# Performance work log

Hardware: AMD Instinct MI355X
Metric: run time of the kernel (lower is better)

## Reference

```python
import jax, jax.numpy as jnp
import numpy as np


def _gru(x, Wih, Whh, bih, bhh):
    # PyTorch GRU cell math, batch=1: x [S, IN], Wih [3H, IN], Whh [3H, H]
    H = Whh.shape[1]
    def step(h, xt):
        gi = Wih @ xt + bih
        gh = Whh @ h + bhh
        i_r, i_z, i_n = jnp.split(gi, 3)
        h_r, h_z, h_n = jnp.split(gh, 3)
        r = jax.nn.sigmoid(i_r + h_r)
        z = jax.nn.sigmoid(i_z + h_z)
        n = jnp.tanh(i_n + r * h_n)
        hn = (1.0 - z) * n + z * h
        return hn, hn
    _, hs = jax.lax.scan(step, jnp.zeros((H,), x.dtype), x)
    return hs  # [S, H]


def setup_inputs() -> dict:
    key = jax.random.key(0)
    ks = jax.random.split(key, 18)
    LOC, TIM, UID = 100000, 48, 5000
    DL, DT, DU, H = 256, 32, 64, 256
    SEQ, NH, TOT, TGT = 2048, 4096, 16384, 1024
    IN = DL + DT  # 288
    s = 0.02
    return {
        "loc": jax.random.randint(ks[0], (SEQ,), 0, LOC),
        "tim": jax.random.randint(ks[1], (SEQ,), 0, TIM),
        "history_loc": jax.random.randint(ks[2], (TOT,), 0, LOC),
        "history_tim": jax.random.randint(ks[3], (TOT,), 0, TIM),
        "history_count": jnp.full((NH,), TOT // NH, dtype=jnp.int32),
        "uid": jax.random.randint(ks[4], (1,), 0, UID),
        "target_len": TGT,
        "emb_loc": jax.random.normal(ks[5], (LOC, DL), jnp.float32) * s,
        "emb_tim": jax.random.normal(ks[6], (TIM, DT), jnp.float32) * s,
        "emb_uid": jax.random.normal(ks[7], (UID, DU), jnp.float32) * s,
        "W_attn": jax.random.normal(ks[8], (2 * H, IN), jnp.float32) * s,
        "b_attn": jnp.zeros((2 * H,), jnp.float32),
        "Wih_f": jax.random.normal(ks[9], (3 * H, IN), jnp.float32) * s,
        "Whh_f": jax.random.normal(ks[10], (3 * H, H), jnp.float32) * s,
        "bih_f": jnp.zeros((3 * H,), jnp.float32),
        "bhh_f": jnp.zeros((3 * H,), jnp.float32),
        "Wih_b": jax.random.normal(ks[11], (3 * H, IN), jnp.float32) * s,
        "Whh_b": jax.random.normal(ks[12], (3 * H, H), jnp.float32) * s,
        "bih_b": jnp.zeros((3 * H,), jnp.float32),
        "bhh_b": jnp.zeros((3 * H,), jnp.float32),
        "Wf": jax.random.normal(ks[13], (LOC, 4 * H + DU), jnp.float32) * s,
        "bf": jnp.zeros((LOC,), jnp.float32),
    }


def reference(loc, tim, history_loc, history_tim, history_count, uid, target_len,
              emb_loc, emb_tim, emb_uid, W_attn, b_attn,
              Wih_f, Whh_f, bih_f, bhh_f, Wih_b, Whh_b, bih_b, bhh_b, Wf, bf):
    counts = np.asarray(jax.device_get(history_count))  # static ragged structure
    n = counts.shape[0]
    seg = jnp.asarray(np.repeat(np.arange(n), counts))
    offs = jnp.asarray(np.concatenate([[0], np.cumsum(counts)[:-1]]))

    # current trajectory embedding [S, IN] (dropout is identity in eval)
    x = jnp.concatenate([emb_loc[loc], emb_tim[tim]], axis=1)

    # ragged segment mean of history loc embeddings; first tim embedding per group
    le = emb_loc[history_loc]  # [TOT, DL]
    loc_mean = jax.ops.segment_sum(le, seg, num_segments=n) / counts.astype(le.dtype)[:, None]
    tim_first = emb_tim[history_tim][offs]  # [n, DT]
    history = jnp.tanh(jnp.concatenate([loc_mean, tim_first], axis=1) @ W_attn.T + b_attn)  # [n, 2H]

    # bidirectional GRU, batch 1
    hf = _gru(x, Wih_f, Whh_f, bih_f, bhh_f)
    hb = _gru(x[::-1], Wih_b, Whh_b, bih_b, bhh_b)[::-1]
    out_state = jnp.concatenate([hf, hb], axis=1)  # [S, 2H]

    q = out_state[-target_len:]                      # [T, 2H]
    attn = jax.nn.softmax(q @ history.T, axis=1)     # dot-product attention
    context = attn @ history                         # [T, 2H]

    uid_emb = jnp.broadcast_to(emb_uid[uid], (target_len, emb_uid.shape[1]))
    out = jnp.concatenate([q, context, uid_emb], axis=1)  # [T, 4H+DU]
    return jax.nn.log_softmax(out @ Wf.T + bf, axis=1)    # [T, LOC]
```

## Files before the change

kernel.cpp:

```cpp
#include <hip/hip_runtime.h>
#include <hip/hip_bf16.h>
#include <stdint.h>

typedef unsigned int uint;
typedef unsigned short ushort;

#define SEQ   2048
#define TGT   1024
#define HDIM  256
#define IN3   288
#define G3    768
#define NHIST 4096
#define DL    256
#define DT    32
#define DU    64
#define NLOC  100000
#define DOUT  1088

typedef short short8 __attribute__((ext_vector_type(8)));
typedef float floatx4 __attribute__((ext_vector_type(4)));
typedef float float4v __attribute__((ext_vector_type(4)));
typedef ushort ushort8v __attribute__((ext_vector_type(8)));
typedef _Float16 half8v __attribute__((ext_vector_type(8)));

__device__ __forceinline__ ushort f2bf(float f) {
  uint u = __builtin_bit_cast(uint, f);
  u += 0x7FFFu + ((u >> 16) & 1u);
  return (ushort)(u >> 16);
}

__global__ void k_pack_whh(const float* __restrict__ whf, const float* __restrict__ whb,
                           uint4* __restrict__ wpack) {
  int idx = blockIdx.x * 256 + threadIdx.x;
  int dir = idx / 24576;
  int r = idx - dir * 24576;
  int wave = r / 3072;
  int r2 = r - wave * 3072;
  int rt = r2 / 512;
  int r3 = r2 - rt * 512;
  int kt = r3 / 64;
  int lane = r3 - kt * 64;
  int row = wave * 96 + rt * 16 + (lane & 15);
  int kb = kt * 32 + (lane >> 4) * 8;
  const float* W = dir ? whb : whf;
  const float* src = W + (size_t)row * 256 + kb;
  half8v h;
  #pragma unroll
  for (int j = 0; j < 8; ++j) h[j] = (_Float16)src[j];
  wpack[idx] = __builtin_bit_cast(uint4, h);
}

__global__ void k_embed_x(const int* __restrict__ loc, const int* __restrict__ tim,
                          const float* __restrict__ emb_loc, const float* __restrict__ emb_tim,
                          ushort* __restrict__ xb) {
  int t = blockIdx.x;
  int tid = threadIdx.x;
  int l = loc[t], m = tim[t];
  if (tid < 256) xb[(size_t)t * IN3 + tid] = f2bf(emb_loc[(size_t)l * DL + tid]);
  if (tid < 32)  xb[(size_t)t * IN3 + 256 + tid] = f2bf(emb_tim[m * DT + tid]);
}

__global__ void k_scan(const int* __restrict__ counts, int* __restrict__ offs) {
  __shared__ int sd[1024];
  int tid = threadIdx.x;
  int base = tid * 4;
  int c0 = counts[base], c1 = counts[base + 1], c2 = counts[base + 2], c3 = counts[base + 3];
  int tot = c0 + c1 + c2 + c3;
  sd[tid] = tot;
  __syncthreads();
  int val = tot;
  for (int off = 1; off < 1024; off <<= 1) {
    int v = (tid >= off) ? sd[tid - off] : 0;
    __syncthreads();
    val += v;
    sd[tid] = val;
    __syncthreads();
  }
  int excl = val - tot;
  offs[base] = excl;
  offs[base + 1] = excl + c0;
  offs[base + 2] = excl + c0 + c1;
  offs[base + 3] = excl + c0 + c1 + c2;
}

__global__ void k_hin(const int* __restrict__ hloc, const int* __restrict__ htim,
                      const int* __restrict__ counts, const int* __restrict__ offs,
                      const float* __restrict__ emb_loc, const float* __restrict__ emb_tim,
                      ushort* __restrict__ hin) {
  int i = blockIdx.x;
  int tid = threadIdx.x;
  int off = offs[i], cnt = counts[i];
  float4v s = {0.f, 0.f, 0.f, 0.f};
  for (int e = 0; e < cnt; ++e) {
    int l = hloc[off + e];
    const float4v* row = (const float4v*)(emb_loc + (size_t)l * DL);
    s += row[tid];
  }
  float inv = 1.f / (float)cnt;
  size_t b = (size_t)i * IN3 + tid * 4;
  hin[b + 0] = f2bf(s[0] * inv);
  hin[b + 1] = f2bf(s[1] * inv);
  hin[b + 2] = f2bf(s[2] * inv);
  hin[b + 3] = f2bf(s[3] * inv);
  if (tid < 32) {
    int ht = htim[off];
    hin[(size_t)i * IN3 + 256 + tid] = f2bf(emb_tim[ht * DT + tid]);
  }
}

template<bool BF32, int ACT>
__global__ __launch_bounds__(256, 2)
void k_gemm(const ushort* __restrict__ A, const void* __restrict__ Bv,
            const float* __restrict__ bias, float* __restrict__ C,
            int M, int N, int K) {
  __shared__ __align__(16) ushort As[128 * 40];
  __shared__ __align__(16) ushort Bs[128 * 40];
  const int tid = threadIdx.x;
  const int m0 = blockIdx.x * 128;
  const int n0 = blockIdx.y * 128;
  const int wave = tid >> 6, lane = tid & 63;
  const int wm = (wave & 1) << 6, wn = (wave >> 1) << 6;
  const int r16 = lane & 15, kq = lane >> 4;
  floatx4 acc[4][4];
  for (int i = 0; i < 4; i++)
    for (int j = 0; j < 4; j++)
      acc[i][j] = (floatx4){0.f, 0.f, 0.f, 0.f};
  const int srow = tid >> 1;
  const int scol = (tid & 1) << 4;
  const bool bok = (n0 + srow) < N;
  for (int k0 = 0; k0 < K; k0 += 32) {
    const ushort* ap = A + (size_t)(m0 + srow) * K + k0 + scol;
    uint4 a0 = *(const uint4*)ap;
    uint4 a1 = *(const uint4*)(ap + 8);
    *(uint4*)&As[srow * 40 + scol] = a0;
    *(uint4*)&As[srow * 40 + scol + 8] = a1;
    if (BF32) {
      const float* bp = (const float*)Bv + (size_t)(n0 + srow) * K + k0 + scol;
      float4v b0 = {0,0,0,0}, b1 = {0,0,0,0}, b2 = {0,0,0,0}, b3 = {0,0,0,0};
      if (bok) {
        b0 = ((const float4v*)bp)[0];
        b1 = ((const float4v*)bp)[1];
        b2 = ((const float4v*)bp)[2];
        b3 = ((const float4v*)bp)[3];
      }
      ushort8v v0, v1;
      for (int j = 0; j < 4; j++) {
        v0[j] = f2bf(b0[j]); v0[4 + j] = f2bf(b1[j]);
        v1[j] = f2bf(b2[j]); v1[4 + j] = f2bf(b3[j]);
      }
      *(ushort8v*)&Bs[srow * 40 + scol] = v0;
      *(ushort8v*)&Bs[srow * 40 + scol + 8] = v1;
    } else {
      const ushort* bp = (const ushort*)Bv + (size_t)(n0 + srow) * K + k0 + scol;
      uint4 z = {0u, 0u, 0u, 0u};
      uint4 b0 = bok ? *(const uint4*)bp : z;
      uint4 b1 = bok ? *(const uint4*)(bp + 8) : z;
      *(uint4*)&Bs[srow * 40 + scol] = b0;
      *(uint4*)&Bs[srow * 40 + scol + 8] = b1;
    }
    __syncthreads();
    short8 af[4], bfr[4];
    #pragma unroll
    for (int i = 0; i < 4; i++) af[i] = *(const short8*)&As[(wm + i * 16 + r16) * 40 + kq * 8];
    #pragma unroll
    for (int i = 0; i < 4; i++) bfr[i] = *(const short8*)&Bs[(wn + i * 16 + r16) * 40 + kq * 8];
    #pragma unroll
    for (int i = 0; i < 4; i++)
      #pragma unroll
      for (int j = 0; j < 4; j++)
        acc[i][j] = __builtin_amdgcn_mfma_f32_16x16x32_bf16(af[i], bfr[j], acc[i][j], 0, 0, 0);
    __syncthreads();
  }
  #pragma unroll
  for (int j = 0; j < 4; j++) {
    int col = n0 + wn + j * 16 + r16;
    if (col >= N) continue;
    float bv = bias ? bias[col] : 0.f;
    #pragma unroll
    for (int i = 0; i < 4; i++) {
      #pragma unroll
      for (int r = 0; r < 4; r++) {
        int row = m0 + wm + i * 16 + kq * 4 + r;
        float v = acc[i][j][r] + bv;
        if (ACT == 1) v = tanhf(v);
        C[(size_t)row * N + col] = v;
      }
    }
  }
}

__global__ void k_hist_cast(const float* __restrict__ Hf, ushort* __restrict__ Hb,
                            ushort* __restrict__ HTb) {
  __shared__ float tle[64][65];
  int i0 = blockIdx.x * 64;
  int j0 = blockIdx.y * 64;
  int tid = threadIdx.x;
  #pragma unroll
  for (int rep = 0; rep < 16; ++rep) {
    int idx = rep * 256 + tid;
    int r = idx >> 6, c = idx & 63;
    float v = Hf[(size_t)(i0 + r) * 512 + j0 + c];
    tle[r][c] = v;
    Hb[(size_t)(i0 + r) * 512 + j0 + c] = f2bf(v);
  }
  __syncthreads();
  #pragma unroll
  for (int rep = 0; rep < 16; ++rep) {
    int idx = rep * 256 + tid;
    int r = idx >> 6, c = idx & 63;
    HTb[(size_t)(j0 + r) * 4096 + i0 + c] = f2bf(tle[c][r]);
  }
}

__global__ __launch_bounds__(512, 2)
void k_gru(const float* __restrict__ gi_f, const float* __restrict__ gi_b,
           const uint4* __restrict__ wpack,
           const float* __restrict__ bhh_f, const float* __restrict__ bhh_b,
           ushort* __restrict__ qb) {
  const int dir = blockIdx.x;
  const int tid = threadIdx.x;
  const int wave = tid >> 6, lane = tid & 63;
  const float* gi = dir ? gi_b : gi_f;
  const float* bhh = dir ? bhh_b : bhh_f;

  __shared__ __align__(16) _Float16 hbuf[256];
  __shared__ __align__(16) _Float16 zbuf[256];
  __shared__ __align__(16) float ghs[768];

  half8v afr[6][8];
  {
    const uint4* wp = wpack + (size_t)dir * 24576 + wave * 3072 + lane;
    #pragma unroll
    for (int rt = 0; rt < 6; ++rt)
      #pragma unroll
      for (int kt = 0; kt < 8; ++kt)
        afr[rt][kt] = __builtin_bit_cast(half8v, wp[rt * 512 + kt * 64]);
  }
  if (tid < 256) { hbuf[tid] = (_Float16)0.f; zbuf[tid] = (_Float16)0.f; }

  const _Float16* bsrc = ((lane & 15) == 0) ? (hbuf + (lane >> 4) * 8) : zbuf;
  const int gw_row = wave * 96 + (lane >> 4) * 4;
  const bool gw_ok = ((lane & 15) == 0);

  const int dim = tid;
  float b_r = 0.f, b_z = 0.f, b_n = 0.f;
  float gi0 = 0.f, gi1 = 0.f, gi2 = 0.f;
  if (tid < 256) {
    b_r = bhh[dim]; b_z = bhh[256 + dim]; b_n = bhh[512 + dim];
    int t0 = dir ? 2047 : 0;
    gi0 = gi[(size_t)t0 * 768 + dim];
    gi1 = gi[(size_t)t0 * 768 + 256 + dim];
    gi2 = gi[(size_t)t0 * 768 + 512 + dim];
  }
  float h_cur = 0.f;
  __syncthreads();

  for (int s = 0; s < 2048; ++s) {
    int tn = dir ? (2046 - s) : (s + 1);
    tn = tn < 0 ? 0 : (tn > 2047 ? 2047 : tn);
    float ngi0 = 0.f, ngi1 = 0.f, ngi2 = 0.f;
    if (tid < 256) {
      ngi0 = gi[(size_t)tn * 768 + dim];
      ngi1 = gi[(size_t)tn * 768 + 256 + dim];
      ngi2 = gi[(size_t)tn * 768 + 512 + dim];
    }

    floatx4 acc[6];
    #pragma unroll
    for (int rt = 0; rt < 6; ++rt) acc[rt] = (floatx4){0.f, 0.f, 0.f, 0.f};
    #pragma unroll
    for (int kt = 0; kt < 8; ++kt) {
      half8v b = *(const half8v*)(bsrc + kt * 32);
      #pragma unroll
      for (int rt = 0; rt < 6; ++rt)
        acc[rt] = __builtin_amdgcn_mfma_f32_16x16x32_f16(afr[rt][kt], b, acc[rt], 0, 0, 0);
    }
    if (gw_ok) {
      #pragma unroll
      for (int rt = 0; rt < 6; ++rt)
        *(floatx4*)&ghs[gw_row + rt * 16] = acc[rt];
    }
    __syncthreads();

    if (tid < 256) {
      float gr = ghs[dim] + b_r + gi0;
      float gz = ghs[256 + dim] + b_z + gi1;
      float gn = ghs[512 + dim] + b_n;
      float r = 1.f / (1.f + __expf(-gr));
      float z = 1.f / (1.f + __expf(-gz));
      float x = gi2 + r * gn;
      float nn = 1.f - 2.f / (__expf(2.f * x) + 1.f);
      h_cur = (1.f - z) * nn + z * h_cur;
      hbuf[dim] = (_Float16)h_cur;
      if (dir == 0) {
        if (s >= 1024) qb[(size_t)(s - 1024) * 512 + dim] = f2bf(h_cur);
      } else {
        if (s < 1024) qb[(size_t)(1023 - s) * 512 + 256 + dim] = f2bf(h_cur);
      }
    }
    __syncthreads();
    gi0 = ngi0; gi1 = ngi1; gi2 = ngi2;
  }
}

__global__ void k_softmax(const float* __restrict__ S, ushort* __restrict__ P) {
  int m = blockIdx.x;
  int tid = threadIdx.x;
  const float* row = S + (size_t)m * 4096;
  float ev[16];
  float mx = -3.0e38f;
  #pragma unroll
  for (int i = 0; i < 16; i++) {
    float x = row[tid + i * 256];
    ev[i] = x;
    mx = fmaxf(mx, x);
  }
  #pragma unroll
  for (int o = 32; o > 0; o >>= 1) mx = fmaxf(mx, __shfl_xor(mx, o));
  __shared__ float red[4];
  __shared__ float red2[4];
  int w = tid >> 6, l = tid & 63;
  if (l == 0) red[w] = mx;
  __syncthreads();
  mx = fmaxf(fmaxf(red[0], red[1]), fmaxf(red[2], red[3]));
  float sm = 0.f;
  #pragma unroll
  for (int i = 0; i < 16; i++) {
    ev[i] = __expf(ev[i] - mx);
    sm += ev[i];
  }
  #pragma unroll
  for (int o = 32; o > 0; o >>= 1) sm += __shfl_xor(sm, o);
  if (l == 0) red2[w] = sm;
  __syncthreads();
  sm = red2[0] + red2[1] + red2[2] + red2[3];
  float inv = 1.f / sm;
  #pragma unroll
  for (int i = 0; i < 16; i++)
    P[(size_t)m * 4096 + tid + i * 256] = f2bf(ev[i] * inv);
}

__global__ void k_assemble(const ushort* __restrict__ qb, const float* __restrict__ ctx,
                           const float* __restrict__ emb_uid, const int* __restrict__ uid,
                           ushort* __restrict__ ob) {
  int m = blockIdx.x, tid = threadIdx.x;
  int u = uid[0];
  for (int c = tid; c < DOUT; c += 256) {
    ushort v;
    if (c < 512) v = qb[(size_t)m * 512 + c];
    else if (c < 1024) v = f2bf(ctx[(size_t)m * 512 + (c - 512)]);
    else v = f2bf(emb_uid[(size_t)u * DU + (c - 1024)]);
    ob[(size_t)m * DOUT + c] = v;
  }
}

__global__ void k_lse(const float* __restrict__ logits, float* __restrict__ lse) {
  int m = blockIdx.x, tid = threadIdx.x;
  const float* row = logits + (size_t)m * NLOC;
  float mx = -3.0e38f, sm = 0.f;
  for (int c = tid; c < NLOC; c += 256) {
    float x = row[c];
    float nm = fmaxf(mx, x);
    sm = sm * __expf(mx - nm) + __expf(x - nm);
    mx = nm;
  }
  #pragma unroll
  for (int o = 32; o > 0; o >>= 1) {
    float omx = __shfl_xor(mx, o);
    float osm = __shfl_xor(sm, o);
    float nm = fmaxf(mx, omx);
    sm = sm * __expf(mx - nm) + osm * __expf(omx - nm);
    mx = nm;
  }
  __shared__ float smx[4], ssm[4];
  int w = tid >> 6;
  if ((tid & 63) == 0) { smx[w] = mx; ssm[w] = sm; }
  __syncthreads();
  if (tid == 0) {
    float M = fmaxf(fmaxf(smx[0], smx[1]), fmaxf(smx[2], smx[3]));
    float S = ssm[0] * __expf(smx[0] - M) + ssm[1] * __expf(smx[1] - M)
            + ssm[2] * __expf(smx[2] - M) + ssm[3] * __expf(smx[3] - M);
    lse[m] = M + logf(S);
  }
}

__global__ void k_sub(float* __restrict__ out, const float* __restrict__ lse) {
  int i = blockIdx.x * 256 + threadIdx.x;
  if (i >= TGT * (NLOC / 4)) return;
  int rowq = i / (NLOC / 4);
  float4v v = ((float4v*)out)[i];
  float l = lse[rowq];
  v[0] -= l; v[1] -= l; v[2] -= l; v[3] -= l;
  ((float4v*)out)[i] = v;
}

extern "C" void kernel_launch(void* const* d_in, const int* in_sizes, int n_in,
                              void* d_out, int out_size, void* d_ws, size_t ws_size,
                              hipStream_t stream) {
  const int*   loc     = (const int*)d_in[0];
  const int*   tim     = (const int*)d_in[1];
  const int*   hloc    = (const int*)d_in[2];
  const int*   htim    = (const int*)d_in[3];
  const int*   hcnt    = (const int*)d_in[4];
  const int*   uid     = (const int*)d_in[5];
  const float* emb_loc = (const float*)d_in[7];
  const float* emb_tim = (const float*)d_in[8];
  const float* emb_uid = (const float*)d_in[9];
  const float* W_attn  = (const float*)d_in[10];
  const float* b_attn  = (const float*)d_in[11];
  const float* Wih_f   = (const float*)d_in[12];
  const float* Whh_f   = (const float*)d_in[13];
  const float* bih_f   = (const float*)d_in[14];
  const float* bhh_f   = (const float*)d_in[15];
  const float* Wih_b   = (const float*)d_in[16];
  const float* Whh_b   = (const float*)d_in[17];
  const float* bih_b   = (const float*)d_in[18];
  const float* bhh_b   = (const float*)d_in[19];
  const float* Wf      = (const float*)d_in[20];
  const float* bfv     = (const float*)d_in[21];
  float* out = (float*)d_out;

  char* w = (char*)d_ws;
  size_t o = 0;
  auto take = [&](size_t bytes) -> void* {
    o = (o + 511) & ~(size_t)511;
    void* p = w + o;
    o += bytes;
    return p;
  };
  int*    offs   = (int*)take(4096 * 4);
  ushort* xb     = (ushort*)take((size_t)SEQ * IN3 * 2);
  ushort* hin    = (ushort*)take((size_t)NHIST * IN3 * 2);
  float*  gi_f   = (float*)take((size_t)SEQ * G3 * 4);
  float*  gi_b   = (float*)take((size_t)SEQ * G3 * 4);
  uint4*  wpack  = (uint4*)take((size_t)49152 * sizeof(uint4));
  float*  hist   = (float*)take((size_t)NHIST * 512 * 4);
  ushort* histb  = (ushort*)take((size_t)NHIST * 512 * 2);
  ushort* histTb = (ushort*)take((size_t)512 * NHIST * 2);
  ushort* qb     = (ushort*)take((size_t)TGT * 512 * 2);
  float*  scores = (float*)take((size_t)TGT * NHIST * 4);
  ushort* attnb  = (ushort*)take((size_t)TGT * NHIST * 2);
  float*  ctx    = (float*)take((size_t)TGT * 512 * 4);
  ushort* ob     = (ushort*)take((size_t)TGT * DOUT * 2);
  float*  lsebuf = (float*)take((size_t)TGT * 4);

  k_pack_whh<<<192, 256, 0, stream>>>(Whh_f, Whh_b, wpack);
  k_embed_x<<<SEQ, 256, 0, stream>>>(loc, tim, emb_loc, emb_tim, xb);
  k_scan<<<1, 1024, 0, stream>>>(hcnt, offs);
  k_hin<<<NHIST, 64, 0, stream>>>(hloc, htim, hcnt, offs, emb_loc, emb_tim, hin);

  k_gemm<true, 0><<<dim3(16, 6), 256, 0, stream>>>(xb, (const void*)Wih_f, bih_f, gi_f, SEQ, G3, IN3);
  k_gemm<true, 0><<<dim3(16, 6), 256, 0, stream>>>(xb, (const void*)Wih_b, bih_b, gi_b, SEQ, G3, IN3);

  k_gemm<true, 1><<<dim3(32, 4), 256, 0, stream>>>(hin, (const void*)W_attn, b_attn, hist, NHIST, 512, IN3);
  k_hist_cast<<<dim3(64, 8), 256, 0, stream>>>(hist, histb, histTb);

  k_gru<<<2, 512, 0, stream>>>(gi_f, gi_b, wpack, bhh_f, bhh_b, qb);

  k_gemm<false, 0><<<dim3(8, 32), 256, 0, stream>>>(qb, (const void*)histb, nullptr, scores, TGT, NHIST, 512);
  k_softmax<<<TGT, 256, 0, stream>>>(scores, attnb);
  k_gemm<false, 0><<<dim3(8, 4), 256, 0, stream>>>(attnb, (const void*)histTb, nullptr, ctx, TGT, 512, NHIST);

  k_assemble<<<TGT, 256, 0, stream>>>(qb, ctx, emb_uid, uid, ob);
  k_gemm<true, 0><<<dim3(8, 782), 256, 0, stream>>>(ob, (const void*)Wf, bfv, out, TGT, NLOC, DOUT);

  k_lse<<<TGT, 256, 0, stream>>>(out, lsebuf);
  k_sub<<<(TGT * (NLOC / 4) + 255) / 256, 256, 0, stream>>>(out, lsebuf);
}
```

Measured before the change: 4.355 ms.

## Shrink GRU block to 4 waves with 12 row tiles each, prefetch gi two steps ahead

The recurrent GRU kernel now runs with 256 threads (4 waves) per direction instead of 512. Each wave keeps 12 register-resident f16 Whh row tiles instead of 6, and the packing kernel is rewritten to match. Every thread now does gate math, so the tid<256 idle branch is gone, and gi is prefetched two timesteps ahead. The aim is cheaper per-step barriers and better latency hiding on the serial chain. The cost is twice the MFMA work per wave and far higher register pressure (96 half8 fragments per thread), which may spill.

```diff
diff --git a/kernel.cpp b/kernel.cpp
--- a/kernel.cpp
+++ b/kernel.cpp
@@ -34,13 +34,13 @@
   int idx = blockIdx.x * 256 + threadIdx.x;
   int dir = idx / 24576;
   int r = idx - dir * 24576;
-  int wave = r / 3072;
-  int r2 = r - wave * 3072;
+  int wave = r / 6144;
+  int r2 = r - wave * 6144;
   int rt = r2 / 512;
   int r3 = r2 - rt * 512;
   int kt = r3 / 64;
   int lane = r3 - kt * 64;
-  int row = wave * 96 + rt * 16 + (lane & 15);
+  int row = wave * 192 + rt * 16 + (lane & 15);
   int kb = kt * 32 + (lane >> 4) * 8;
   const float* W = dir ? whb : whf;
   const float* src = W + (size_t)row * 256 + kb;
@@ -212,7 +212,7 @@
   }
 }
 
-__global__ __launch_bounds__(512, 2)
+__global__ __launch_bounds__(256, 1)
 void k_gru(const float* __restrict__ gi_f, const float* __restrict__ gi_b,
            const uint4* __restrict__ wpack,
            const float* __restrict__ bhh_f, const float* __restrict__ bhh_b,
@@ -227,68 +227,67 @@
   __shared__ __align__(16) _Float16 zbuf[256];
   __shared__ __align__(16) float ghs[768];
 
-  half8v afr[6][8];
+  half8v afr[12][8];
   {
-    const uint4* wp = wpack + (size_t)dir * 24576 + wave * 3072 + lane;
-    #pragma unroll
-    for (int rt = 0; rt < 6; ++rt)
+    const uint4* wp = wpack + (size_t)dir * 24576 + wave * 6144 + lane;
+    #pragma unroll
+    for (int rt = 0; rt < 12; ++rt)
       #pragma unroll
       for (int kt = 0; kt < 8; ++kt)
         afr[rt][kt] = __builtin_bit_cast(half8v, wp[rt * 512 + kt * 64]);
   }
-  if (tid < 256) { hbuf[tid] = (_Float16)0.f; zbuf[tid] = (_Float16)0.f; }
+  hbuf[tid] = (_Float16)0.f;
+  zbuf[tid] = (_Float16)0.f;
 
   const _Float16* bsrc = ((lane & 15) == 0) ? (hbuf + (lane >> 4) * 8) : zbuf;
-  const int gw_row = wave * 96 + (lane >> 4) * 4;
+  const int gw_row = wave * 192 + (lane >> 4) * 4;
   const bool gw_ok = ((lane & 15) == 0);
 
   const int dim = tid;
-  float b_r = 0.f, b_z = 0.f, b_n = 0.f;
-  float gi0 = 0.f, gi1 = 0.f, gi2 = 0.f;
-  if (tid < 256) {
-    b_r = bhh[dim]; b_z = bhh[256 + dim]; b_n = bhh[512 + dim];
-    int t0 = dir ? 2047 : 0;
-    gi0 = gi[(size_t)t0 * 768 + dim];
-    gi1 = gi[(size_t)t0 * 768 + 256 + dim];
-    gi2 = gi[(size_t)t0 * 768 + 512 + dim];
-  }
+  const float b_r = bhh[dim], b_z = bhh[256 + dim], b_n = bhh[512 + dim];
+
+  int ta = dir ? 2047 : 0;
+  int tb = dir ? 2046 : 1;
+  float c0 = gi[(size_t)ta * 768 + dim];
+  float c1 = gi[(size_t)ta * 768 + 256 + dim];
+  float c2 = gi[(size_t)ta * 768 + 512 + dim];
+  float n0v = gi[(size_t)tb * 768 + dim];
+  float n1v = gi[(size_t)tb * 768 + 256 + dim];
+  float n2v = gi[(size_t)tb * 768 + 512 + dim];
   float h_cur = 0.f;
   __syncthreads();
 
   for (int s = 0; s < 2048; ++s) {
-    int tn = dir ? (2046 - s) : (s + 1);
-    tn = tn < 0 ? 0 : (tn > 2047 ? 2047 : tn);
-    float ngi0 = 0.f, ngi1 = 0.f, ngi2 = 0.f;
-    if (tid < 256) {
-      ngi0 = gi[(size_t)tn * 768 + dim];
-      ngi1 = gi[(size_t)tn * 768 + 256 + dim];
-      ngi2 = gi[(size_t)tn * 768 + 512 + dim];
-    }
-
-    floatx4 acc[6];
-    #pragma unroll
-    for (int rt = 0; rt < 6; ++rt) acc[rt] = (floatx4){0.f, 0.f, 0.f, 0.f};
+    int t2 = dir ? (2045 - s) : (s + 2);
+    t2 = t2 < 0 ? 0 : (t2 > 2047 ? 2047 : t2);
+    float p0 = gi[(size_t)t2 * 768 + dim];
+    float p1 = gi[(size_t)t2 * 768 + 256 + dim];
+    float p2 = gi[(size_t)t2 * 768 + 512 + dim];
+
+    floatx4 acc[12];
+    #pragma unroll
+    for (int rt = 0; rt < 12; ++rt) acc[rt] = (floatx4){0.f, 0.f, 0.f, 0.f};
     #pragma unroll
     for (int kt = 0; kt < 8; ++kt) {
       half8v b = *(const half8v*)(bsrc + kt * 32);
       #pragma unroll
-      for (int rt = 0; rt < 6; ++rt)
+      for (int rt = 0; rt < 12; ++rt)
         acc[rt] = __builtin_amdgcn_mfma_f32_16x16x32_f16(afr[rt][kt], b, acc[rt], 0, 0, 0);
     }
     if (gw_ok) {
       #pragma unroll
-      for (int rt = 0; rt < 6; ++rt)
+      for (int rt = 0; rt < 12; ++rt)
         *(floatx4*)&ghs[gw_row + rt * 16] = acc[rt];
     }
     __syncthreads();
 
-    if (tid < 256) {
-      float gr = ghs[dim] + b_r + gi0;
-      float gz = ghs[256 + dim] + b_z + gi1;
+    {
+      float gr = ghs[dim] + b_r + c0;
+      float gz = ghs[256 + dim] + b_z + c1;
       float gn = ghs[512 + dim] + b_n;
       float r = 1.f / (1.f + __expf(-gr));
       float z = 1.f / (1.f + __expf(-gz));
-      float x = gi2 + r * gn;
+      float x = c2 + r * gn;
       float nn = 1.f - 2.f / (__expf(2.f * x) + 1.f);
       h_cur = (1.f - z) * nn + z * h_cur;
       hbuf[dim] = (_Float16)h_cur;
@@ -299,7 +298,8 @@
       }
     }
     __syncthreads();
-    gi0 = ngi0; gi1 = ngi1; gi2 = ngi2;
+    c0 = n0v; c1 = n1v; c2 = n2v;
+    n0v = p0; n1v = p1; n2v = p2;
   }
 }
 
@@ -455,7 +455,7 @@
   k_gemm<true, 1><<<dim3(32, 4), 256, 0, stream>>>(hin, (const void*)W_attn, b_attn, hist, NHIST, 512, IN3);
   k_hist_cast<<<dim3(64, 8), 256, 0, stream>>>(hist, histb, histTb);
 
-  k_gru<<<2, 512, 0, stream>>>(gi_f, gi_b, wpack, bhh_f, bhh_b, qb);
+  k_gru<<<2, 256, 0, stream>>>(gi_f, gi_b, wpack, bhh_f, bhh_b, qb);
 
   k_gemm<false, 0><<<dim3(8, 32), 256, 0, stream>>>(qb, (const void*)histb, nullptr, scores, TGT, NHIST, 512);
   k_softmax<<<TGT, 256, 0, stream>>>(scores, attnb);
```

Result: slower. 5.134 ms (+17.9%).
